# Kernel tuning notes

Hardware: AMD Instinct MI355X
Metric: run time of the kernel (lower is better)

Reference implementation:

```python
import jax, jax.numpy as jnp
import numpy as np
from jax import lax

N, S, H, L, E, V = 10000, 20, 512, 2, 100000, 10000


def setup_inputs() -> dict:
    key = jax.random.key(0)
    ks = jax.random.split(key, 12)
    return {
        "emb": jax.random.normal(ks[0], (V, H), jnp.float32),
        "W_ir": jax.random.normal(ks[1], (L, H, H), jnp.float32) * (2.0 / H) ** 0.5,
        "b_ir": jnp.ones((L, H), jnp.float32),
        "W_iz": jax.random.normal(ks[2], (L, H, H), jnp.float32) * (2.0 / H) ** 0.5,
        "b_iz": jnp.ones((L, H), jnp.float32),
        "lin_w": jax.random.normal(ks[3], (1, H), jnp.float32) * (1.0 / H) ** 0.5,
        "lin_b": jnp.zeros((1,), jnp.float32),
        "skip_w": jax.random.uniform(ks[4], (H, H), jnp.float32),
        "skip_b": jax.random.uniform(ks[5], (H,), jnp.float32),
        "walk_idx": jax.random.randint(ks[6], (N, S), 0, V),
        "edge_label_index": jax.random.randint(ks[7], (2, E), 0, N),
    }


def reference(emb, W_ir, b_ir, W_iz, b_iz, lin_w, lin_b, skip_w, skip_b,
              walk_idx, edge_label_index):
    x = emb[walk_idx]                       # [N, S, H]
    hn = jnp.zeros((x.shape[0], emb.shape[1]), x.dtype)
    for l in range(W_ir.shape[0]):
        # gates depend only on x, precompute all steps: F.linear(x, W) = x @ W.T
        h_all = jnp.einsum('nsh,kh->snk', x, W_ir[l]) + b_ir[l]          # [S, N, H]
        z_all = jax.nn.sigmoid(jnp.einsum('nsh,kh->snk', x, W_iz[l]) + b_iz[l])

        def step(h, tz):
            ht, zt = tz
            return (1.0 - zt) * h + zt * ht, None

        hn, _ = lax.scan(step, hn, (h_all, z_all))
    # note: F.dropout result in original is dead (overwritten); omitted
    score = jax.nn.sigmoid(hn @ lin_w.T + lin_b)        # [N, 1]
    node_feat = score[edge_label_index]                  # [2, E, 1]
    pred = jnp.sum(node_feat[0] * node_feat[1], axis=-1)  # [E] ('dot' decode)
    out2 = hn @ skip_w.T + skip_b                        # [N, H]
    return pred, out2
```

## Files before the change

### kernel.cpp

```cpp
#include <hip/hip_runtime.h>

#define H  512
#define NN 10000
#define SS 20
#define VV 100000
#define EE 100000

typedef __bf16 bf16x8 __attribute__((ext_vector_type(8)));
typedef float  f32x4  __attribute__((ext_vector_type(4)));

__device__ __forceinline__ unsigned short f2bf(float f) {
  unsigned u = __builtin_bit_cast(unsigned, f);
  u += 0x7FFFu + ((u >> 16) & 1u);
  return (unsigned short)(u >> 16);
}
__device__ __forceinline__ float bflo(int x) {
  return __builtin_bit_cast(float, (unsigned)x << 16);
}
__device__ __forceinline__ float bfhi(int x) {
  return __builtin_bit_cast(float, (unsigned)x & 0xFFFF0000u);
}
__device__ __forceinline__ float sigm(float x) { return 1.f / (1.f + __expf(-x)); }

__device__ __forceinline__ unsigned pk(float lo, float hi) {
  unsigned a = __builtin_bit_cast(unsigned, lo) + 0x8000u;
  unsigned b = __builtin_bit_cast(unsigned, hi) + 0x8000u;
  return __builtin_amdgcn_perm(b, a, 0x07060302u);
}
__device__ __forceinline__ void cvt_store8(unsigned short* dst, float4 a, float4 b) {
  int4 v;
  v.x = (int)pk(a.x, a.y); v.y = (int)pk(a.z, a.w);
  v.z = (int)pk(b.x, b.y); v.w = (int)pk(b.z, b.w);
  *(int4*)dst = v;
}
__device__ __forceinline__ bf16x8 cvt8(float4 a, float4 b) {
  int4 v;
  v.x = (int)pk(a.x, a.y); v.y = (int)pk(a.z, a.w);
  v.z = (int)pk(b.x, b.y); v.w = (int)pk(b.z, b.w);
  return __builtin_bit_cast(bf16x8, v);
}

__launch_bounds__(256, 2)
__global__ void gru_fused(const float* __restrict__ emb,
                          const float* __restrict__ W_ir,
                          const float* __restrict__ W_iz,
                          const float* __restrict__ b_ir,
                          const float* __restrict__ b_iz,
                          const int* __restrict__ walk,
                          unsigned short* __restrict__ hnb) {
  __shared__ unsigned short As[2][80 * 64];
  __shared__ unsigned short hout[2][4][32];

  const int tid = threadIdx.x;
  const int w = tid >> 6, lane = tid & 63;
  const int r = lane & 15, q = lane >> 4;
  const int c0 = blockIdx.x * 32;

  const int ly = r & 1;
  const int cch = c0 + 8 * w + (r >> 1);
  bf16x8 barr[2][16];
  float bias2[2];
  #pragma unroll
  for (int t = 0; t < 2; ++t) {
    const float* wrow = (t ? W_iz : W_ir) + (long)ly * H * H + (long)cch * H;
    #pragma unroll
    for (int u = 0; u < 16; ++u) {
      const float* s = wrow + u * 32 + q * 8;
      barr[t][u] = cvt8(*(const float4*)s, *(const float4*)(s + 4));
    }
    bias2[t] = (t ? b_iz : b_ir)[ly * H + cch];
  }

  const int row0 = tid >> 3, g0 = tid & 7;
  const int row1 = row0 + 32, row2 = row0 + 64;
  const bool has2 = (tid < 128);
  #define LMAP(m) (20 * (((m) >> 2) & 3) + 4 * ((m) >> 4) + ((m) & 3))
  #define SWZ(m)  ((m) * 64 + ((g0 ^ ((m) & 7)) * 8))
  const int L0 = LMAP(row0), L1 = LMAP(row1), L2 = LMAP(row2);
  const int sw0 = SWZ(row0), sw1 = SWZ(row1), sw2 = SWZ(row2);

  const int sb = blockIdx.y;
  const int ngA = (2500 * sb) >> 6;
  const int ngB = (2500 * (sb + 1)) >> 6;

  int v0 = walk[ngA * 80 + L0]; v0 = ((unsigned)v0 < VV) ? v0 : 0;
  int v1 = walk[ngA * 80 + L1]; v1 = ((unsigned)v1 < VV) ? v1 : 0;
  int cur0 = v0 * H, cur1 = v1 * H, cur2 = 0;
  if (has2) { int v2 = walk[ngA * 80 + L2]; v2 = ((unsigned)v2 < VV) ? v2 : 0; cur2 = v2 * H; }

  float4 pa0, pb0, pa1, pb1, pa2 = {0,0,0,0}, pb2 = {0,0,0,0};
  {
    const float* s0 = emb + cur0 + g0 * 8;
    pa0 = *(const float4*)s0; pb0 = *(const float4*)(s0 + 4);
    const float* s1 = emb + cur1 + g0 * 8;
    pa1 = *(const float4*)s1; pb1 = *(const float4*)(s1 + 4);
    if (has2) { const float* s2 = emb + cur2 + g0 * 8;
                pa2 = *(const float4*)s2; pb2 = *(const float4*)(s2 + 4); }
  }

  f32x4 acc[5][2];
  const f32x4 fz = {0.f, 0.f, 0.f, 0.f};

  for (int ng = ngA; ng < ngB; ++ng) {
    #pragma unroll
    for (int mt = 0; mt < 5; ++mt)
      #pragma unroll
      for (int t = 0; t < 2; ++t) acc[mt][t] = fz;

    const int ngn = (ng + 1 < ngB) ? ng + 1 : ng;
    int n0 = walk[ngn * 80 + L0]; n0 = ((unsigned)n0 < VV) ? n0 : 0;
    int n1 = walk[ngn * 80 + L1]; n1 = ((unsigned)n1 < VV) ? n1 : 0;
    const int nxt0 = n0 * H, nxt1 = n1 * H;
    int nxt2 = 0;
    if (has2) { int n2 = walk[ngn * 80 + L2]; n2 = ((unsigned)n2 < VV) ? n2 : 0; nxt2 = n2 * H; }

    #pragma unroll
    for (int kc = 0; kc < 8; ++kc) {
      unsigned short* Ab = &As[kc & 1][0];
      cvt_store8(&Ab[sw0], pa0, pb0);
      cvt_store8(&Ab[sw1], pa1, pb1);
      if (has2) cvt_store8(&Ab[sw2], pa2, pb2);
      __syncthreads();
      {
        const int ko = (kc < 7) ? (kc + 1) * 64 : 0;
        const int o0 = (kc < 7) ? cur0 : nxt0;
        const int o1 = (kc < 7) ? cur1 : nxt1;
        const int o2 = (kc < 7) ? cur2 : nxt2;
        const float* s0 = emb + o0 + ko + g0 * 8;
        pa0 = *(const float4*)s0; pb0 = *(const float4*)(s0 + 4);
        const float* s1 = emb + o1 + ko + g0 * 8;
        pa1 = *(const float4*)s1; pb1 = *(const float4*)(s1 + 4);
        if (has2) { const float* s2 = emb + o2 + ko + g0 * 8;
                    pa2 = *(const float4*)s2; pb2 = *(const float4*)(s2 + 4); }
      }
      #pragma unroll
      for (int ks = 0; ks < 2; ++ks) {
        bf16x8 a[5];
        #pragma unroll
        for (int mt = 0; mt < 5; ++mt) {
          const int ar = mt * 16 + r;
          a[mt] = *(const bf16x8*)&Ab[ar * 64 + (((ks * 4 + q) ^ (ar & 7)) * 8)];
        }
        #pragma unroll
        for (int mt = 0; mt < 5; ++mt)
          #pragma unroll
          for (int t = 0; t < 2; ++t)
            acc[mt][t] = __builtin_amdgcn_mfma_f32_16x16x32_bf16(
                a[mt], barr[t][kc * 2 + ks], acc[mt][t], 0, 0, 0);
      }
    }

    {
      float hn1 = 0.f, a2 = 1.f, b2 = 0.f;
      #pragma unroll
      for (int s = 0; s < 20; ++s) {
        const float yh = acc[s >> 2][0][s & 3] + bias2[0];
        const float yz = acc[s >> 2][1][s & 3] + bias2[1];
        const float z = sigm(yz);
        hn1 += z * (yh - hn1);
        a2 *= (1.f - z);
        b2 += z * (yh - b2);
      }
      const float u2 = __shfl_xor(hn1, 1);
      if (ly == 1) hout[ng & 1][q][8 * w + (r >> 1)] = f2bf(a2 * u2 + b2);
    }
    __syncthreads();
    if (tid < 16) {
      const int nd = tid >> 2, seg = tid & 3;
      int4 v = *(const int4*)&hout[ng & 1][nd][seg * 8];
      *(int4*)(hnb + (long)(ng * 4 + nd) * 1024 + c0 + seg * 8) = v;
    }
    cur0 = nxt0; cur1 = nxt1; cur2 = nxt2;
  }
}

__global__ void score_kernel(const unsigned short* __restrict__ hnb,
                             const float* __restrict__ lin_w,
                             const float* __restrict__ lin_b,
                             float* __restrict__ R) {
  int tid = threadIdx.x;
  int wv = tid >> 6, lane = tid & 63;
  int node = blockIdx.x * 4 + wv;
  int k = lane * 8;
  int4 hv = *(const int4*)(hnb + (long)node * 1024 + k);
  float4 w0 = *(const float4*)(lin_w + k);
  float4 w1 = *(const float4*)(lin_w + k + 4);
  float s = bflo(hv.x) * w0.x + bfhi(hv.x) * w0.y + bflo(hv.y) * w0.z + bfhi(hv.y) * w0.w
          + bflo(hv.z) * w1.x + bfhi(hv.z) * w1.y + bflo(hv.w) * w1.z + bfhi(hv.w) * w1.w;
  #pragma unroll
  for (int off = 32; off > 0; off >>= 1) s += __shfl_down(s, off);
  if (lane == 0) R[256 + (long)node * 512] = sigm(s + lin_b[0]);
}

__global__ void pred_kernel(const int* __restrict__ eli, const float* __restrict__ R,
                            float* __restrict__ out) {
  int e = blockIdx.x * 256 + threadIdx.x;
  if (e < EE) {
    int a = eli[e];       a = (unsigned)a < NN ? a : 0;
    int b = eli[EE + e];  b = (unsigned)b < NN ? b : 0;
    out[e] = R[256 + (long)a * 512] * R[256 + (long)b * 512];
  }
}

__launch_bounds__(256)
__global__ void out2_kernel(const unsigned short* __restrict__ hnb,
                            const float* __restrict__ skip_w,
                            const float* __restrict__ skip_b,
                            float* __restrict__ out2) {
  __shared__ unsigned short Asl[32][520];
  __shared__ unsigned short Bsl[512][40];
  const int tid = threadIdx.x;
  const int lane = tid & 63, wv = tid >> 6;
  const int r = lane & 15, q = lane >> 4;
  const int m0 = blockIdx.x * 32;

  {
    int arow = tid >> 4;
    int acol = (tid & 15) * 32;
    #pragma unroll
    for (int hh = 0; hh < 2; ++hh) {
      int grow = m0 + hh * 16 + arow;
      unsigned short* dst = &Asl[hh * 16 + arow][acol];
      if (grow < NN) {
        const unsigned short* hr = hnb + (long)grow * 1024 + acol;
        *(int4*)(dst)      = *(const int4*)(hr);
        *(int4*)(dst + 8)  = *(const int4*)(hr + 8);
        *(int4*)(dst + 16) = *(const int4*)(hr + 16);
        *(int4*)(dst + 24) = *(const int4*)(hr + 24);
      } else {
        int4 z = {0, 0, 0, 0};
        *(int4*)(dst) = z; *(int4*)(dst + 8) = z;
        *(int4*)(dst + 16) = z; *(int4*)(dst + 24) = z;
      }
    }
  }

  const f32x4 fzero = {0.f, 0.f, 0.f, 0.f};
  f32x4 acc[2][8];
  #pragma unroll
  for (int rg = 0; rg < 2; ++rg)
    #pragma unroll
    for (int i = 0; i < 8; ++i) acc[rg][i] = fzero;

  const int ksub = (tid & 3) * 8;
  const int jb = tid >> 2;

  for (int k0 = 0; k0 < H; k0 += 32) {
    __syncthreads();
    #pragma unroll
    for (int it = 0; it < 8; ++it) {
      int jj = it * 64 + jb;
      const float* src = skip_w + (long)jj * H + k0 + ksub;
      cvt_store8(&Bsl[jj][ksub], *(const float4*)src, *(const float4*)(src + 4));
    }
    __syncthreads();
    bf16x8 af0 = *(const bf16x8*)&Asl[r][k0 + q * 8];
    bf16x8 af1 = *(const bf16x8*)&Asl[16 + r][k0 + q * 8];
    #pragma unroll
    for (int i = 0; i < 8; ++i) {
      bf16x8 bf = *(const bf16x8*)&Bsl[(wv * 8 + i) * 16 + r][q * 8];
      acc[0][i] = __builtin_amdgcn_mfma_f32_16x16x32_bf16(af0, bf, acc[0][i], 0, 0, 0);
      acc[1][i] = __builtin_amdgcn_mfma_f32_16x16x32_bf16(af1, bf, acc[1][i], 0, 0, 0);
    }
  }
  #pragma unroll
  for (int rg = 0; rg < 2; ++rg)
    #pragma unroll
    for (int i = 0; i < 8; ++i) {
      int col = (wv * 8 + i) * 16 + r;
      float sbv = skip_b[col];
      #pragma unroll
      for (int g = 0; g < 4; ++g) {
        int grow = m0 + rg * 16 + q * 4 + g;
        if (grow < NN) out2[(long)grow * H + col] = acc[rg][i][g] + sbv;
      }
    }
}

extern "C" void kernel_launch(void* const* d_in, const int* in_sizes, int n_in,
                              void* d_out, int out_size, void* d_ws, size_t ws_size,
                              hipStream_t stream) {
  const float* emb    = (const float*)d_in[0];
  const float* W_ir   = (const float*)d_in[1];
  const float* b_ir   = (const float*)d_in[2];
  const float* W_iz   = (const float*)d_in[3];
  const float* b_iz   = (const float*)d_in[4];
  const float* lin_w  = (const float*)d_in[5];
  const float* lin_b  = (const float*)d_in[6];
  const float* skip_w = (const float*)d_in[7];
  const float* skip_b = (const float*)d_in[8];
  const int*   walk   = (const int*)d_in[9];
  const int*   eli    = (const int*)d_in[10];
  float* out = (float*)d_out;
  float* R   = out + EE;
  unsigned short* hnb = (unsigned short*)R;

  dim3 g1(16, 64);
  gru_fused<<<g1, 256, 0, stream>>>(emb, W_ir, W_iz, b_ir, b_iz, walk, hnb);
  score_kernel<<<2500, 256, 0, stream>>>(hnb, lin_w, lin_b, R);
  pred_kernel<<<391, 256, 0, stream>>>(eli, R, out);
  out2_kernel<<<313, 256, 0, stream>>>(hnb, skip_w, skip_b, R);
}
```

Baseline: 797.8 us.

## Split GRU work across 512-thread blocks with M-tile halves and combine via LDS

Reworks the fused GRU kernel so each block covers 16 output channels instead of 32, using 512 threads. Eight waves split both the channel groups and the 5 M-tiles (3/2 per half), and each lane holds one weight (W_ir or W_iz) rather than both. The two halves' scan results are combined as affine (a,b) pairs through shared memory, and block IDs are remapped so blocks sharing a node range are grouped. This cuts per-thread register pressure and raises occupancy, at the cost of twice the emb gather traffic per node group, extra shuffles, and uneven MFMA work between the two wave halves.

```diff
diff --git a/kernel.cpp b/kernel.cpp
--- a/kernel.cpp
+++ b/kernel.cpp
@@ -40,7 +40,7 @@
   return __builtin_bit_cast(bf16x8, v);
 }
 
-__launch_bounds__(256, 2)
+__launch_bounds__(512, 4)
 __global__ void gru_fused(const float* __restrict__ emb,
                           const float* __restrict__ W_ir,
                           const float* __restrict__ W_iz,
@@ -49,128 +49,134 @@
                           const int* __restrict__ walk,
                           unsigned short* __restrict__ hnb) {
   __shared__ unsigned short As[2][80 * 64];
-  __shared__ unsigned short hout[2][4][32];
+  __shared__ float2 cmb[2][2][4][16];
 
   const int tid = threadIdx.x;
   const int w = tid >> 6, lane = tid & 63;
   const int r = lane & 15, q = lane >> 4;
-  const int c0 = blockIdx.x * 32;
-
-  const int ly = r & 1;
-  const int cch = c0 + 8 * w + (r >> 1);
-  bf16x8 barr[2][16];
-  float bias2[2];
-  #pragma unroll
-  for (int t = 0; t < 2; ++t) {
-    const float* wrow = (t ? W_iz : W_ir) + (long)ly * H * H + (long)cch * H;
+  const int cgl = w & 3, mthalf = w >> 2;
+  const int p = r & 1, ly = (r >> 1) & 1, chl = r >> 2;
+
+  const int hwid = blockIdx.y * 32 + blockIdx.x;
+  const int cg = (hwid >> 3) & 31;
+  const int sb = ((hwid & 7) << 3) + (hwid >> 8);
+  const int c0 = cg * 16;
+
+  const int cch = c0 + cgl * 4 + chl;
+  bf16x8 barr[16];
+  float bias;
+  {
+    const float* wrow = (p ? W_iz : W_ir) + (long)ly * H * H + (long)cch * H;
     #pragma unroll
     for (int u = 0; u < 16; ++u) {
       const float* s = wrow + u * 32 + q * 8;
-      barr[t][u] = cvt8(*(const float4*)s, *(const float4*)(s + 4));
-    }
-    bias2[t] = (t ? b_iz : b_ir)[ly * H + cch];
+      barr[u] = cvt8(*(const float4*)s, *(const float4*)(s + 4));
+    }
+    bias = (p ? b_iz : b_ir)[ly * H + cch];
   }
 
   const int row0 = tid >> 3, g0 = tid & 7;
-  const int row1 = row0 + 32, row2 = row0 + 64;
-  const bool has2 = (tid < 128);
+  const bool has1 = (tid < 128);
+  const int row1 = 64 + ((tid >> 3) & 15);
   #define LMAP(m) (20 * (((m) >> 2) & 3) + 4 * ((m) >> 4) + ((m) & 3))
   #define SWZ(m)  ((m) * 64 + ((g0 ^ ((m) & 7)) * 8))
-  const int L0 = LMAP(row0), L1 = LMAP(row1), L2 = LMAP(row2);
-  const int sw0 = SWZ(row0), sw1 = SWZ(row1), sw2 = SWZ(row2);
-
-  const int sb = blockIdx.y;
+  const int L0 = LMAP(row0), L1 = LMAP(row1);
+  const int sw0 = SWZ(row0), sw1 = SWZ(row1);
+
+  const int mtb = mthalf * 3;
+  const int nmt = 3 - mthalf;
+  const int abase = (mtb * 16 + r) * 64;
+  const int sxo0 = ((q) ^ (r & 7)) * 8;
+  const int sxo1 = ((4 + q) ^ (r & 7)) * 8;
+
   const int ngA = (2500 * sb) >> 6;
   const int ngB = (2500 * (sb + 1)) >> 6;
 
   int v0 = walk[ngA * 80 + L0]; v0 = ((unsigned)v0 < VV) ? v0 : 0;
-  int v1 = walk[ngA * 80 + L1]; v1 = ((unsigned)v1 < VV) ? v1 : 0;
-  int cur0 = v0 * H, cur1 = v1 * H, cur2 = 0;
-  if (has2) { int v2 = walk[ngA * 80 + L2]; v2 = ((unsigned)v2 < VV) ? v2 : 0; cur2 = v2 * H; }
-
-  float4 pa0, pb0, pa1, pb1, pa2 = {0,0,0,0}, pb2 = {0,0,0,0};
+  int cur0 = v0 * H, cur1 = 0;
+  if (has1) { int v1 = walk[ngA * 80 + L1]; v1 = ((unsigned)v1 < VV) ? v1 : 0; cur1 = v1 * H; }
+
+  float4 pa0, pb0, pa1 = {0,0,0,0}, pb1 = {0,0,0,0};
   {
     const float* s0 = emb + cur0 + g0 * 8;
     pa0 = *(const float4*)s0; pb0 = *(const float4*)(s0 + 4);
-    const float* s1 = emb + cur1 + g0 * 8;
-    pa1 = *(const float4*)s1; pb1 = *(const float4*)(s1 + 4);
-    if (has2) { const float* s2 = emb + cur2 + g0 * 8;
-                pa2 = *(const float4*)s2; pb2 = *(const float4*)(s2 + 4); }
-  }
-
-  f32x4 acc[5][2];
+    if (has1) { const float* s1 = emb + cur1 + g0 * 8;
+                pa1 = *(const float4*)s1; pb1 = *(const float4*)(s1 + 4); }
+  }
+
+  f32x4 acc[3];
   const f32x4 fz = {0.f, 0.f, 0.f, 0.f};
 
   for (int ng = ngA; ng < ngB; ++ng) {
     #pragma unroll
-    for (int mt = 0; mt < 5; ++mt)
-      #pragma unroll
-      for (int t = 0; t < 2; ++t) acc[mt][t] = fz;
+    for (int j = 0; j < 3; ++j) acc[j] = fz;
 
     const int ngn = (ng + 1 < ngB) ? ng + 1 : ng;
     int n0 = walk[ngn * 80 + L0]; n0 = ((unsigned)n0 < VV) ? n0 : 0;
-    int n1 = walk[ngn * 80 + L1]; n1 = ((unsigned)n1 < VV) ? n1 : 0;
-    const int nxt0 = n0 * H, nxt1 = n1 * H;
-    int nxt2 = 0;
-    if (has2) { int n2 = walk[ngn * 80 + L2]; n2 = ((unsigned)n2 < VV) ? n2 : 0; nxt2 = n2 * H; }
+    const int nxt0 = n0 * H;
+    int nxt1 = 0;
+    if (has1) { int n1 = walk[ngn * 80 + L1]; n1 = ((unsigned)n1 < VV) ? n1 : 0; nxt1 = n1 * H; }
 
     #pragma unroll
     for (int kc = 0; kc < 8; ++kc) {
       unsigned short* Ab = &As[kc & 1][0];
       cvt_store8(&Ab[sw0], pa0, pb0);
-      cvt_store8(&Ab[sw1], pa1, pb1);
-      if (has2) cvt_store8(&Ab[sw2], pa2, pb2);
+      if (has1) cvt_store8(&Ab[sw1], pa1, pb1);
       __syncthreads();
       {
         const int ko = (kc < 7) ? (kc + 1) * 64 : 0;
         const int o0 = (kc < 7) ? cur0 : nxt0;
         const int o1 = (kc < 7) ? cur1 : nxt1;
-        const int o2 = (kc < 7) ? cur2 : nxt2;
         const float* s0 = emb + o0 + ko + g0 * 8;
         pa0 = *(const float4*)s0; pb0 = *(const float4*)(s0 + 4);
-        const float* s1 = emb + o1 + ko + g0 * 8;
-        pa1 = *(const float4*)s1; pb1 = *(const float4*)(s1 + 4);
-        if (has2) { const float* s2 = emb + o2 + ko + g0 * 8;
-                    pa2 = *(const float4*)s2; pb2 = *(const float4*)(s2 + 4); }
+        if (has1) { const float* s1 = emb + o1 + ko + g0 * 8;
+                    pa1 = *(const float4*)s1; pb1 = *(const float4*)(s1 + 4); }
       }
       #pragma unroll
       for (int ks = 0; ks < 2; ++ks) {
-        bf16x8 a[5];
+        const int sx = ks ? sxo1 : sxo0;
         #pragma unroll
-        for (int mt = 0; mt < 5; ++mt) {
-          const int ar = mt * 16 + r;
-          a[mt] = *(const bf16x8*)&Ab[ar * 64 + (((ks * 4 + q) ^ (ar & 7)) * 8)];
+        for (int j = 0; j < 3; ++j) {
+          if (j < nmt) {
+            bf16x8 a = *(const bf16x8*)&Ab[abase + j * 1024 + sx];
+            acc[j] = __builtin_amdgcn_mfma_f32_16x16x32_bf16(
+                a, barr[kc * 2 + ks], acc[j], 0, 0, 0);
+          }
         }
-        #pragma unroll
-        for (int mt = 0; mt < 5; ++mt)
+      }
+    }
+
+    {
+      float aa = 1.f, bb = 0.f;
+      #pragma unroll
+      for (int j = 0; j < 3; ++j) {
+        if (j < nmt) {
           #pragma unroll
-          for (int t = 0; t < 2; ++t)
-            acc[mt][t] = __builtin_amdgcn_mfma_f32_16x16x32_bf16(
-                a[mt], barr[t][kc * 2 + ks], acc[mt][t], 0, 0, 0);
-      }
-    }
-
-    {
-      float hn1 = 0.f, a2 = 1.f, b2 = 0.f;
-      #pragma unroll
-      for (int s = 0; s < 20; ++s) {
-        const float yh = acc[s >> 2][0][s & 3] + bias2[0];
-        const float yz = acc[s >> 2][1][s & 3] + bias2[1];
-        const float z = sigm(yz);
-        hn1 += z * (yh - hn1);
-        a2 *= (1.f - z);
-        b2 += z * (yh - b2);
-      }
-      const float u2 = __shfl_xor(hn1, 1);
-      if (ly == 1) hout[ng & 1][q][8 * w + (r >> 1)] = f2bf(a2 * u2 + b2);
+          for (int i = 0; i < 4; ++i) {
+            const float y = acc[j][i] + bias;
+            const float t = __shfl_xor(y, 1);
+            const float yh = p ? t : y;
+            const float yz = p ? y : t;
+            const float z = sigm(yz);
+            aa *= (1.f - z);
+            bb += z * (yh - bb);
+          }
+        }
+      }
+      if (!p) cmb[mthalf][ly][q][cgl * 4 + chl] = make_float2(aa, bb);
     }
     __syncthreads();
-    if (tid < 16) {
-      const int nd = tid >> 2, seg = tid & 3;
-      int4 v = *(const int4*)&hout[ng & 1][nd][seg * 8];
-      *(int4*)(hnb + (long)(ng * 4 + nd) * 1024 + c0 + seg * 8) = v;
-    }
-    cur0 = nxt0; cur1 = nxt1; cur2 = nxt2;
+    if (tid < 64) {
+      const int ch = tid & 15, nd = tid >> 4;
+      const float2 c0a = cmb[0][0][nd][ch];
+      const float2 c0b = cmb[1][0][nd][ch];
+      const float2 c1a = cmb[0][1][nd][ch];
+      const float2 c1b = cmb[1][1][nd][ch];
+      const float B0 = c0b.x * c0a.y + c0b.y;
+      const float hn = (c1b.x * c1a.x) * B0 + (c1b.x * c1a.y + c1b.y);
+      hnb[(long)(ng * 4 + nd) * 1024 + c0 + ch] = f2bf(hn);
+    }
+    cur0 = nxt0; cur1 = nxt1;
   }
 }
 
@@ -295,8 +301,8 @@
   float* R   = out + EE;
   unsigned short* hnb = (unsigned short*)R;
 
-  dim3 g1(16, 64);
-  gru_fused<<<g1, 256, 0, stream>>>(emb, W_ir, W_iz, b_ir, b_iz, walk, hnb);
+  dim3 g1(32, 64);
+  gru_fused<<<g1, 512, 0, stream>>>(emb, W_ir, W_iz, b_ir, b_iz, walk, hnb);
   score_kernel<<<2500, 256, 0, stream>>>(hnb, lin_w, lin_b, R);
   pred_kernel<<<391, 256, 0, stream>>>(eli, R, out);
   out2_kernel<<<313, 256, 0, stream>>>(hnb, skip_w, skip_b, R);
```

Result: slower. 2.156 ms (+170.3%).

## Halve per-block output channels to cut registers and double GRU grid

Applied to the files above, without the earlier changes.

Each block now covers 16 hidden channels instead of 32. The two gate weights are split across adjacent lanes via shuffles, which halves the B-fragment and accumulator registers so launch bounds can request 3 blocks per SM. The grid doubles to 32x64 with a remapped block id that groups column groups and sample blocks. The per-step shared-memory output staging and its barrier are replaced by direct scattered 2-byte global stores. In exchange, the embedding gather and bf16 conversion traffic is duplicated across twice as many column blocks.

```diff
diff --git a/kernel.cpp b/kernel.cpp
--- a/kernel.cpp
+++ b/kernel.cpp
@@ -40,7 +40,7 @@
   return __builtin_bit_cast(bf16x8, v);
 }
 
-__launch_bounds__(256, 2)
+__launch_bounds__(256, 3)
 __global__ void gru_fused(const float* __restrict__ emb,
                           const float* __restrict__ W_ir,
                           const float* __restrict__ W_iz,
@@ -49,26 +49,29 @@
                           const int* __restrict__ walk,
                           unsigned short* __restrict__ hnb) {
   __shared__ unsigned short As[2][80 * 64];
-  __shared__ unsigned short hout[2][4][32];
 
   const int tid = threadIdx.x;
   const int w = tid >> 6, lane = tid & 63;
   const int r = lane & 15, q = lane >> 4;
-  const int c0 = blockIdx.x * 32;
-
-  const int ly = r & 1;
-  const int cch = c0 + 8 * w + (r >> 1);
-  bf16x8 barr[2][16];
-  float bias2[2];
-  #pragma unroll
-  for (int t = 0; t < 2; ++t) {
-    const float* wrow = (t ? W_iz : W_ir) + (long)ly * H * H + (long)cch * H;
+  const int cgl = w;
+  const int p = r & 1, ly = (r >> 1) & 1, chl = r >> 2;
+
+  const int hwid = blockIdx.y * 32 + blockIdx.x;
+  const int cg = (hwid >> 3) & 31;
+  const int sb = ((hwid & 7) << 3) + (hwid >> 8);
+  const int c0 = cg * 16;
+
+  const int cch = c0 + cgl * 4 + chl;
+  bf16x8 barr[16];
+  float bias;
+  {
+    const float* wrow = (p ? W_iz : W_ir) + (long)ly * H * H + (long)cch * H;
     #pragma unroll
     for (int u = 0; u < 16; ++u) {
       const float* s = wrow + u * 32 + q * 8;
-      barr[t][u] = cvt8(*(const float4*)s, *(const float4*)(s + 4));
-    }
-    bias2[t] = (t ? b_iz : b_ir)[ly * H + cch];
+      barr[u] = cvt8(*(const float4*)s, *(const float4*)(s + 4));
+    }
+    bias = (p ? b_iz : b_ir)[ly * H + cch];
   }
 
   const int row0 = tid >> 3, g0 = tid & 7;
@@ -79,7 +82,6 @@
   const int L0 = LMAP(row0), L1 = LMAP(row1), L2 = LMAP(row2);
   const int sw0 = SWZ(row0), sw1 = SWZ(row1), sw2 = SWZ(row2);
 
-  const int sb = blockIdx.y;
   const int ngA = (2500 * sb) >> 6;
   const int ngB = (2500 * (sb + 1)) >> 6;
 
@@ -98,14 +100,12 @@
                 pa2 = *(const float4*)s2; pb2 = *(const float4*)(s2 + 4); }
   }
 
-  f32x4 acc[5][2];
+  f32x4 acc[5];
   const f32x4 fz = {0.f, 0.f, 0.f, 0.f};
 
   for (int ng = ngA; ng < ngB; ++ng) {
     #pragma unroll
-    for (int mt = 0; mt < 5; ++mt)
-      #pragma unroll
-      for (int t = 0; t < 2; ++t) acc[mt][t] = fz;
+    for (int mt = 0; mt < 5; ++mt) acc[mt] = fz;
 
     const int ngn = (ng + 1 < ngB) ? ng + 1 : ng;
     int n0 = walk[ngn * 80 + L0]; n0 = ((unsigned)n0 < VV) ? n0 : 0;
@@ -143,32 +143,26 @@
         }
         #pragma unroll
         for (int mt = 0; mt < 5; ++mt)
-          #pragma unroll
-          for (int t = 0; t < 2; ++t)
-            acc[mt][t] = __builtin_amdgcn_mfma_f32_16x16x32_bf16(
-                a[mt], barr[t][kc * 2 + ks], acc[mt][t], 0, 0, 0);
+          acc[mt] = __builtin_amdgcn_mfma_f32_16x16x32_bf16(
+              a[mt], barr[kc * 2 + ks], acc[mt], 0, 0, 0);
       }
     }
 
     {
-      float hn1 = 0.f, a2 = 1.f, b2 = 0.f;
+      float aa = 1.f, bb = 0.f;
       #pragma unroll
       for (int s = 0; s < 20; ++s) {
-        const float yh = acc[s >> 2][0][s & 3] + bias2[0];
-        const float yz = acc[s >> 2][1][s & 3] + bias2[1];
+        const float y = acc[s >> 2][s & 3] + bias;
+        const float t = __shfl_xor(y, 1);
+        const float yh = p ? t : y;
+        const float yz = p ? y : t;
         const float z = sigm(yz);
-        hn1 += z * (yh - hn1);
-        a2 *= (1.f - z);
-        b2 += z * (yh - b2);
-      }
-      const float u2 = __shfl_xor(hn1, 1);
-      if (ly == 1) hout[ng & 1][q][8 * w + (r >> 1)] = f2bf(a2 * u2 + b2);
-    }
-    __syncthreads();
-    if (tid < 16) {
-      const int nd = tid >> 2, seg = tid & 3;
-      int4 v = *(const int4*)&hout[ng & 1][nd][seg * 8];
-      *(int4*)(hnb + (long)(ng * 4 + nd) * 1024 + c0 + seg * 8) = v;
+        aa *= (1.f - z);
+        bb += z * (yh - bb);
+      }
+      const float bbo = __shfl_xor(bb, 2);
+      if (ly == 1 && p == 0)
+        hnb[(long)(ng * 4 + q) * 1024 + cch] = f2bf(aa * bbo + bb);
     }
     cur0 = nxt0; cur1 = nxt1; cur2 = nxt2;
   }
@@ -295,7 +289,7 @@
   float* R   = out + EE;
   unsigned short* hnb = (unsigned short*)R;
 
-  dim3 g1(16, 64);
+  dim3 g1(32, 64);
   gru_fused<<<g1, 256, 0, stream>>>(emb, W_ir, W_iz, b_ir, b_iz, walk, hnb);
   score_kernel<<<2500, 256, 0, stream>>>(hnb, lin_w, lin_b, R);
   pred_kernel<<<391, 256, 0, stream>>>(eli, R, out);
```

New measurement: 993.1 us. +24.5%, slower.
